# Optimization experiments

Measured on AMD Instinct MI355X. Metric: run time of the kernel, lower is better.

The kernel has to match this reference:

```python
import jax, jax.numpy as jnp
import numpy as np

T, B, I, H, LBL = 200, 1024, 128, 128, 4


def setup_inputs() -> dict:
    key = jax.random.key(0)
    ks = jax.random.split(key, 14)
    si = 1.0 / np.sqrt(I)
    sh = 1.0 / np.sqrt(H)
    inputs = jax.random.normal(ks[0], (T, B, I), jnp.float32)
    lengths = jnp.maximum(jax.random.randint(ks[1], (B,), 1, T + 1), LBL).astype(jnp.int32)
    return {
        "inputs": inputs,
        "lengths": lengths,
        "Wih_g": jax.random.normal(ks[2], (3 * H, I), jnp.float32) * si,
        "Whh_g": jax.random.normal(ks[3], (3 * H, H), jnp.float32) * sh,
        "bih_g": jax.random.normal(ks[4], (3 * H,), jnp.float32) * sh,
        "bhh_g": jax.random.normal(ks[5], (3 * H,), jnp.float32) * sh,
        "Wih_l": jax.random.normal(ks[6], (3 * H, I), jnp.float32) * si,
        "Whh_l": jax.random.normal(ks[7], (3 * H, H), jnp.float32) * sh,
        "bih_l": jax.random.normal(ks[8], (3 * H,), jnp.float32) * sh,
        "bhh_l": jax.random.normal(ks[9], (3 * H,), jnp.float32) * sh,
        "A1": jax.random.normal(ks[10], (H, H), jnp.float32) * sh,
        "A2": jax.random.normal(ks[11], (H, H), jnp.float32) * sh,
        "v1": jax.random.normal(ks[12], (1, H), jnp.float32) * sh,
        "label_len": LBL,
    }


def gru(x, Wih, Whh, bih, bhh):
    # x: [T, B, I] time-major. PyTorch GRU cell semantics.
    Bq, Hq = x.shape[1], Whh.shape[1]
    gi_all = jnp.einsum('tbi,gi->tbg', x, Wih) + bih  # precompute input projections [T,B,3H]
    def step(h, gi):
        gh = h @ Whh.T + bhh
        ir, iz, inn = jnp.split(gi, 3, axis=-1)
        hr, hz, hn = jnp.split(gh, 3, axis=-1)
        r = jax.nn.sigmoid(ir + hr)
        z = jax.nn.sigmoid(iz + hz)
        n = jnp.tanh(inn + r * hn)
        h = (1.0 - z) * n + z * h
        return h, h
    h0 = jnp.zeros((Bq, Hq), x.dtype)
    _, hs = jax.lax.scan(step, h0, gi_all)
    return hs  # [T, B, H]


def reference(inputs, lengths, Wih_g, Whh_g, bih_g, bhh_g,
              Wih_l, Whh_l, bih_l, bhh_l, A1, A2, v1, label_len):
    h_g = gru(inputs, Wih_g, Whh_g, bih_g, bhh_g)  # [T,B,H]
    h_l = gru(inputs, Wih_l, Whh_l, bih_l, bhh_l)  # [T,B,H]
    # attention score per step s: v1(sigmoid(A1 h_l + A2 h_g)), query-independent
    pre = jax.nn.sigmoid(jnp.einsum('tbh,gh->tbg', h_l, A1) +
                         jnp.einsum('tbh,gh->tbg', h_g, A2))
    scores = jnp.einsum('tbg,og->tbo', pre, v1)  # [T,B,1]
    # per-t output = cumsum_{s<=t}(score*h_l) + h_g[t]
    out = jnp.cumsum(scores * h_l, axis=0) + h_g  # [T,B,H]
    out_b = jnp.transpose(out, (1, 0, 2))  # [B,T,H]
    # gather last label_len timesteps of each sequence: h[b,k] = out[L_b-label_len+k, b]
    idx = lengths[:, None].astype(jnp.int32) - label_len + jnp.arange(label_len, dtype=jnp.int32)[None, :]
    idx = jnp.clip(idx, 0, out_b.shape[1] - 1)  # [B, label_len]
    h = jnp.take_along_axis(out_b, idx[:, :, None], axis=1)  # [B, label_len, H]
    return h
```

## Files before the change

### kernel.cpp

```cpp
#include <hip/hip_runtime.h>
#include <stdint.h>


typedef __attribute__((ext_vector_type(8))) short short8;
typedef __attribute__((ext_vector_type(4))) float float4v;

#define LDS_BARRIER() asm volatile("s_waitcnt lgkmcnt(0)\n\ts_barrier" ::: "memory")

__device__ inline float bf2f(unsigned short u){
  union { unsigned int i; float f; } v; v.i = ((unsigned int)u) << 16; return v.f;
}
__device__ inline unsigned short f2bf(float f){
  union { float f; unsigned int i; } v; v.f = f;
  unsigned int x = v.i;
  return (unsigned short)((x + 0x7fffu + ((x >> 16) & 1u)) >> 16);
}
__device__ inline unsigned int cvt_pk_bf16(float a, float b){
  unsigned int r;
  asm("v_cvt_pk_bf16_f32 %0, %1, %2" : "=v"(r) : "v"(a), "v"(b));
  return r;
}
__device__ inline float sigm(float x){ return __builtin_amdgcn_rcpf(1.0f + __expf(-x)); }

__global__ void k_prep(float* cum, const float* A1, const float* A2, unsigned short* a12,
                       const float* Wih_g, const float* Whh_g,
                       const float* Wih_l, const float* Whh_l, unsigned short* wst)
{
  int i = blockIdx.x * blockDim.x + threadIdx.x;
  if (i < 131072) cum[i] = 0.0f;
  if (i < 32768) a12[i] = f2bf((i < 16384) ? A1[i] : A2[i - 16384]);
  {
    int f = i >> 12;
    int r = i & 4095;
    int t = r >> 3, e = r & 7;
    int l15 = t & 15, q = (t >> 4) & 3, wv = t >> 6;
    int col = wv * 16 + l15;
    int kf = f & 3, g3 = f >> 2;
    int G = g3 % 3, gm = g3 / 3;
    const float* src = (gm == 0) ? Wih_g : (gm == 1) ? Whh_g : (gm == 2) ? Wih_l : Whh_l;
    int row = G * 128 + col;
    int k = kf * 32 + q * 8 + e;
    wst[i] = f2bf(src[(size_t)row * 128 + k]);
  }
}

union __align__(16) LdsU {
  struct { unsigned short hbuf[2][16][136]; unsigned short xbuf[2][16][136]; } scan;
  struct { unsigned short M1[128][136]; unsigned short M2[128][136]; } sc;
  struct { unsigned short hlL[50 * 512]; float scL[4][50]; } cm;
};

__global__ __launch_bounds__(512, 2) void k_fat(
    const float* __restrict__ x,
    const float* __restrict__ bih_g, const float* __restrict__ bhh_g,
    const float* __restrict__ bih_l, const float* __restrict__ bhh_l,
    const unsigned short* __restrict__ wst,
    const unsigned short* __restrict__ a12, const float* __restrict__ v1,
    const int* __restrict__ lengths,
    unsigned short* __restrict__ hl, unsigned short* __restrict__ hg,
    float* __restrict__ score, float* __restrict__ cum, float* __restrict__ out,
    int scan_t0, int score_t0, int cum_t0)
{
  __shared__ LdsU lds;
  int tid = threadIdx.x;
  int bid = blockIdx.x;

  if (bid < 128) {
    if (scan_t0 < 0) return;
    const int tc = 100;
    int t0 = scan_t0;
    auto& hbuf = lds.scan.hbuf;
    auto& xbuf = lds.scan.xbuf;

    int w = tid >> 6, L = tid & 63, l15 = L & 15, q = L >> 4;
    int gru = bid & 1;
    int b0 = (bid >> 1) * 16;
    const float* bih = gru ? bih_l : bih_g;
    const float* bhh = gru ? bhh_l : bhh_g;
    unsigned short* myseq = gru ? hl : hg;

    int col = w * 16 + l15;

    short8 Wi[3][4], Wh[3][4];
    {
      int gmi = gru * 2;
      int gmh = gru * 2 + 1;
      #pragma unroll
      for (int G = 0; G < 3; G++) {
        #pragma unroll
        for (int kf = 0; kf < 4; kf++) {
          Wi[G][kf] = *(const short8*)(wst + (((size_t)((gmi * 3 + G) * 4 + kf)) << 12) + tid * 8);
          Wh[G][kf] = *(const short8*)(wst + (((size_t)((gmh * 3 + G) * 4 + kf)) << 12) + tid * 8);
        }
      }
    }
    float br  = bih[col]       + bhh[col];
    float bz  = bih[128 + col] + bhh[128 + col];
    float bin = bih[256 + col];
    float bnh = bhh[256 + col];

    float hold[4];
    if (t0 == 0) {
      #pragma unroll
      for (int r = 0; r < 4; r++) { hold[r] = 0.0f; hbuf[0][q * 4 + r][col] = 0; }
    } else {
      const unsigned short* carry = myseq + (size_t)(t0 - 1) * 131072;
      #pragma unroll
      for (int r = 0; r < 4; r++) {
        int m = q * 4 + r;
        unsigned short u = carry[(size_t)(b0 + m) * 128 + col];
        hold[r] = bf2f(u);
        hbuf[0][m][col] = u;
      }
    }
    int xrow = tid >> 5, xc4 = (tid & 31) * 4;
    size_t hoff = (size_t)b0 * 128 + xrow * 128 + xc4;
    {
      float4 x0 = ((const float4*)(x + ((size_t)t0 * 1024 + b0) * 128))[tid];
      *(uint2*)&xbuf[0][xrow][xc4] = make_uint2(cvt_pk_bf16(x0.x, x0.y), cvt_pk_bf16(x0.z, x0.w));
    }
    float4 xr = ((const float4*)(x + ((size_t)(t0 + 1) * 1024 + b0) * 128))[tid];
    __syncthreads();

    float4v cx0 = (float4v){0.f,0.f,0.f,0.f}, cx1 = cx0, cx2 = cx0;
    {
      short8 Ax[4];
      #pragma unroll
      for (int kf = 0; kf < 4; kf++) Ax[kf] = *(const short8*)&xbuf[0][l15][kf * 32 + q * 8];
      #pragma unroll
      for (int kf = 0; kf < 4; kf++) cx0 = __builtin_amdgcn_mfma_f32_16x16x32_bf16(Ax[kf], Wi[0][kf], cx0, 0,0,0);
      #pragma unroll
      for (int kf = 0; kf < 4; kf++) cx1 = __builtin_amdgcn_mfma_f32_16x16x32_bf16(Ax[kf], Wi[1][kf], cx1, 0,0,0);
      #pragma unroll
      for (int kf = 0; kf < 4; kf++) cx2 = __builtin_amdgcn_mfma_f32_16x16x32_bf16(Ax[kf], Wi[2][kf], cx2, 0,0,0);
    }
    *(uint2*)&xbuf[1][xrow][xc4] = make_uint2(cvt_pk_bf16(xr.x, xr.y), cvt_pk_bf16(xr.z, xr.w));
    xr = ((const float4*)(x + ((size_t)(t0 + 2) * 1024 + b0) * 128))[tid];
    LDS_BARRIER();

    auto step = [&](int s, int pin, int pout) {
      short8 Ah[4], Axn[4];
      #pragma unroll
      for (int kf = 0; kf < 4; kf++) Ah[kf]  = *(const short8*)&hbuf[pin][l15][kf * 32 + q * 8];
      #pragma unroll
      for (int kf = 0; kf < 4; kf++) Axn[kf] = *(const short8*)&xbuf[pout][l15][kf * 32 + q * 8];

      if (s > 0) {
        uint2 hv = *(const uint2*)&hbuf[pin][xrow][xc4];
        *(uint2*)(myseq + (size_t)(t0 + s - 1) * 131072 + hoff) = hv;
      }

      float4v rh = (float4v){0.f,0.f,0.f,0.f}, zh = rh, nh = rh;
      #pragma unroll
      for (int kf = 0; kf < 4; kf++) rh = __builtin_amdgcn_mfma_f32_16x16x32_bf16(Ah[kf], Wh[0][kf], rh, 0,0,0);
      #pragma unroll
      for (int kf = 0; kf < 4; kf++) zh = __builtin_amdgcn_mfma_f32_16x16x32_bf16(Ah[kf], Wh[1][kf], zh, 0,0,0);
      #pragma unroll
      for (int kf = 0; kf < 4; kf++) nh = __builtin_amdgcn_mfma_f32_16x16x32_bf16(Ah[kf], Wh[2][kf], nh, 0,0,0);

      float4v nx0 = (float4v){0.f,0.f,0.f,0.f}, nx1 = nx0, nx2 = nx0;
      #pragma unroll
      for (int kf = 0; kf < 4; kf++) nx0 = __builtin_amdgcn_mfma_f32_16x16x32_bf16(Axn[kf], Wi[0][kf], nx0, 0,0,0);
      #pragma unroll
      for (int kf = 0; kf < 4; kf++) nx1 = __builtin_amdgcn_mfma_f32_16x16x32_bf16(Axn[kf], Wi[1][kf], nx1, 0,0,0);
      #pragma unroll
      for (int kf = 0; kf < 4; kf++) nx2 = __builtin_amdgcn_mfma_f32_16x16x32_bf16(Axn[kf], Wi[2][kf], nx2, 0,0,0);

      *(uint2*)&xbuf[pin][xrow][xc4] = make_uint2(cvt_pk_bf16(xr.x, xr.y), cvt_pk_bf16(xr.z, xr.w));
      {
        int t3 = t0 + (s + 3 < tc ? s + 3 : tc - 1);
        xr = ((const float4*)(x + ((size_t)t3 * 1024 + b0) * 128))[tid];
      }

      float cr[4], cz[4], cn[4];
      #pragma unroll
      for (int r = 0; r < 4; r++) { cr[r] = cx0[r] + br; cz[r] = cx1[r] + bz; cn[r] = cx2[r] + bin; }

      float hnv[4];
      #pragma unroll
      for (int r = 0; r < 4; r++) {
        float er = __expf(-(rh[r] + cr[r]));
        float ez = __expf(-(zh[r] + cz[r]));
        float pr = 1.0f + er, pz = 1.0f + ez;
        float inv = __builtin_amdgcn_rcpf(pr * pz);
        float rr = pz * inv;
        float zz = pr * inv;
        float y  = cn[r] + rr * (nh[r] + bnh);
        float em = __expf(-2.0f * y);
        float nn = 2.0f * __builtin_amdgcn_rcpf(1.0f + em) - 1.0f;
        hnv[r] = nn + zz * (hold[r] - nn);
        hold[r] = hnv[r];
      }
      unsigned int p01 = cvt_pk_bf16(hnv[0], hnv[1]);
      unsigned int p23 = cvt_pk_bf16(hnv[2], hnv[3]);
      hbuf[pout][q * 4 + 0][col] = (unsigned short)p01;
      hbuf[pout][q * 4 + 1][col] = (unsigned short)(p01 >> 16);
      hbuf[pout][q * 4 + 2][col] = (unsigned short)p23;
      hbuf[pout][q * 4 + 3][col] = (unsigned short)(p23 >> 16);

      cx0 = nx0; cx1 = nx1; cx2 = nx2;
      LDS_BARRIER();
    };

    for (int s = 0; s + 1 < tc; s += 2) { step(s, 0, 1); step(s + 1, 1, 0); }
    {
      uint2 hv = *(const uint2*)&hbuf[tc & 1][xrow][xc4];
      *(uint2*)(myseq + (size_t)(t0 + tc - 1) * 131072 + hoff) = hv;
    }
    return;
  }

  if (bid < 328) {
    if (score_t0 < 0) return;
    int rb = bid - 128;
    int w = tid >> 6, L = tid & 63;
    int l15 = L & 15, q = L >> 4;
    int s = score_t0 + (rb >> 1);
    int bhalf = (rb & 1) * 512;
    auto& M1 = lds.sc.M1;
    auto& M2 = lds.sc.M2;

    #pragma unroll
    for (int it = 0; it < 4; it++) {
      int f8 = it * 512 + tid;
      *(short8*)&M1[f8 >> 4][(f8 & 15) * 8] = *(const short8*)(a12 + (size_t)f8 * 8);
      *(short8*)&M2[f8 >> 4][(f8 & 15) * 8] = *(const short8*)(a12 + 16384 + (size_t)f8 * 8);
    }
    __syncthreads();

    float v1v[8];
    #pragma unroll
    for (int nt = 0; nt < 8; nt++) v1v[nt] = v1[nt * 16 + l15];

    short8 Fl[4], Fg[4], Pl[4], Pg[4];
    {
      size_t base = ((size_t)s * 1024 + bhalf + (size_t)w * 16 + l15) * 128;
      #pragma unroll
      for (int kf = 0; kf < 4; kf++) {
        Fl[kf] = *(const short8*)(hl + base + kf * 32 + q * 8);
        Fg[kf] = *(const short8*)(hg + base + kf * 32 + q * 8);
      }
    }
    #pragma unroll
    for (int it = 0; it < 4; it++) {
      int b0s = bhalf + (it * 8 + w) * 16;
      if (it + 1 < 4) {
        size_t base = ((size_t)s * 1024 + bhalf + (size_t)((it + 1) * 8 + w) * 16 + l15) * 128;
        #pragma unroll
        for (int kf = 0; kf < 4; kf++) {
          Pl[kf] = *(const short8*)(hl + base + kf * 32 + q * 8);
          Pg[kf] = *(const short8*)(hg + base + kf * 32 + q * 8);
        }
      }
      float4v acc[8];
      #pragma unroll
      for (int nt = 0; nt < 8; nt++) {
        float4v a = (float4v){0.f, 0.f, 0.f, 0.f};
        #pragma unroll
        for (int kf = 0; kf < 4; kf++)
          a = __builtin_amdgcn_mfma_f32_16x16x32_bf16(
              Fl[kf], *(const short8*)&M1[nt * 16 + l15][kf * 32 + q * 8], a, 0, 0, 0);
        #pragma unroll
        for (int kf = 0; kf < 4; kf++)
          a = __builtin_amdgcn_mfma_f32_16x16x32_bf16(
              Fg[kf], *(const short8*)&M2[nt * 16 + l15][kf * 32 + q * 8], a, 0, 0, 0);
        acc[nt] = a;
      }
      float p4[4];
      #pragma unroll
      for (int r = 0; r < 4; r++) {
        float sum = 0.f;
        #pragma unroll
        for (int nt = 0; nt < 8; nt++) sum += v1v[nt] * sigm(acc[nt][r]);
        sum += __shfl_xor(sum, 1, 16);
        sum += __shfl_xor(sum, 2, 16);
        sum += __shfl_xor(sum, 4, 16);
        sum += __shfl_xor(sum, 8, 16);
        p4[r] = sum;
      }
      if (l15 == 0) {
        #pragma unroll
        for (int r = 0; r < 4; r++)
          score[(size_t)(b0s + q * 4 + r) * 200 + s] = p4[r];
      }
      #pragma unroll
      for (int kf = 0; kf < 4; kf++) { Fl[kf] = Pl[kf]; Fg[kf] = Pg[kf]; }
    }
    return;
  }

  if (cum_t0 < 0) return;
  {
    int rb = bid - 328;
    int b4 = tid >> 7, j = tid & 127;
    int b0c = rb * 4;
    int b = b0c + b4;
    int base = b4 * 128 + j;

    float c = cum[(size_t)b * 128 + j];
    int cap0 = lengths[b] - 4;

    for (int seg = 0; seg < 2; seg++) {
      int t0s = cum_t0 + seg * 50;
      __syncthreads();

      float hgv[4];
      #pragma unroll
      for (int d = 0; d < 4; d++) {
        int sl = cap0 + d - t0s;
        hgv[d] = (sl >= 0 && sl < 50) ? bf2f(hg[((size_t)(cap0 + d) * 1024 + b) * 128 + j]) : 0.f;
      }

      for (int f8 = tid; f8 < 50 * 64; f8 += 512) {
        int sl = f8 >> 6, r8 = f8 & 63;
        *(short8*)&lds.cm.hlL[(size_t)f8 * 8] =
            *(const short8*)(hl + ((size_t)(t0s + sl) * 1024 + b0c) * 128 + r8 * 8);
      }
      for (int i = tid; i < 4 * 50; i += 512) {
        int bb = i / 50, sl = i - bb * 50;
        lds.cm.scL[bb][sl] = score[(size_t)(b0c + bb) * 200 + t0s + sl];
      }
      __syncthreads();

      for (int sl = 0; sl < 50; sl += 5) {
        float h[5], scv[5];
        #pragma unroll
        for (int k = 0; k < 5; k++) {
          h[k] = bf2f(lds.cm.hlL[(size_t)(sl + k) * 512 + base]);
          scv[k] = lds.cm.scL[b4][sl + k];
        }
        #pragma unroll
        for (int k = 0; k < 5; k++) {
          c += scv[k] * h[k];
          int d = (t0s + sl + k) - cap0;
          if ((unsigned)d < 4u)
            out[((size_t)b * 4 + d) * 128 + j] = c + hgv[d];
        }
      }
    }
    cum[(size_t)b * 128 + j] = c;
  }
}

extern "C" void kernel_launch(void* const* d_in, const int* in_sizes, int n_in,
                              void* d_out, int out_size, void* d_ws, size_t ws_size,
                              hipStream_t stream)
{
  const float* x     = (const float*)d_in[0];
  const int* lengths = (const int*)d_in[1];
  const float* Wih_g = (const float*)d_in[2];
  const float* Whh_g = (const float*)d_in[3];
  const float* bih_g = (const float*)d_in[4];
  const float* bhh_g = (const float*)d_in[5];
  const float* Wih_l = (const float*)d_in[6];
  const float* Whh_l = (const float*)d_in[7];
  const float* bih_l = (const float*)d_in[8];
  const float* bhh_l = (const float*)d_in[9];
  const float* A1    = (const float*)d_in[10];
  const float* A2    = (const float*)d_in[11];
  const float* v1    = (const float*)d_in[12];
  float* out = (float*)d_out;

  char* wsb = (char*)d_ws;
  size_t o = 0;
  unsigned short* a12 = (unsigned short*)(wsb + o); o += 65536;
  float* cum          = (float*)(wsb + o);          o += 524288;
  unsigned short* wst = (unsigned short*)(wsb + o); o += 393216;
  unsigned short* hl  = (unsigned short*)(wsb + o); o += (size_t)200 * 1024 * 128 * 2;
  unsigned short* hg  = (unsigned short*)(wsb + o); o += (size_t)200 * 1024 * 128 * 2;
  float* score        = (float*)(wsb + o);          o += (size_t)1024 * 200 * 4;
  if (o > ws_size) return;

  k_prep<<<768, 256, 0, stream>>>(cum, A1, A2, a12, Wih_g, Whh_g, Wih_l, Whh_l, wst);

  k_fat<<<128, 512, 0, stream>>>(x, bih_g, bhh_g, bih_l, bhh_l, wst, a12, v1, lengths,
                                 hl, hg, score, cum, out, 0, -1, -1);
  k_fat<<<328, 512, 0, stream>>>(x, bih_g, bhh_g, bih_l, bhh_l, wst, a12, v1, lengths,
                                 hl, hg, score, cum, out, 100, 0, -1);
  k_fat<<<584, 512, 0, stream>>>(x, bih_g, bhh_g, bih_l, bhh_l, wst, a12, v1, lengths,
                                 hl, hg, score, cum, out, -1, 100, 0);
  k_fat<<<584, 512, 0, stream>>>(x, bih_g, bhh_g, bih_l, bhh_l, wst, a12, v1, lengths,
                                 hl, hg, score, cum, out, -1, -1, 100);
}
```

Measured before the change: 398.8 us.

## Fuse attention score into cumsum blocks and drop separate score pass

Computes attention scores inside the cumsum blocks with MFMA on hl/hg tiles staged in LDS, removing the separate score kernel stage and the global score buffer. The pipeline shrinks from four k_fat launches to three, and the cumsum for t<100 now overlaps with the second half of the scan. The first scan launch converts fp32 weights to bf16 in registers itself, so it no longer waits on the prep kernel for its weights. A dead 'build' branch is left in, and hg is now read twice (score and staging), adding LDS traffic per cum block.

New measurement: 398.6 us. Within noise of the previous version (-0.0%).

```diff
diff --git a/kernel.cpp b/kernel.cpp
--- a/kernel.cpp
+++ b/kernel.cpp
@@ -22,51 +22,33 @@
 }
 __device__ inline float sigm(float x){ return __builtin_amdgcn_rcpf(1.0f + __expf(-x)); }
 
-__global__ void k_prep(float* cum, const float* A1, const float* A2, unsigned short* a12,
-                       const float* Wih_g, const float* Whh_g,
-                       const float* Wih_l, const float* Whh_l, unsigned short* wst)
-{
-  int i = blockIdx.x * blockDim.x + threadIdx.x;
-  if (i < 131072) cum[i] = 0.0f;
-  if (i < 32768) a12[i] = f2bf((i < 16384) ? A1[i] : A2[i - 16384]);
-  {
-    int f = i >> 12;
-    int r = i & 4095;
-    int t = r >> 3, e = r & 7;
-    int l15 = t & 15, q = (t >> 4) & 3, wv = t >> 6;
-    int col = wv * 16 + l15;
-    int kf = f & 3, g3 = f >> 2;
-    int G = g3 % 3, gm = g3 / 3;
-    const float* src = (gm == 0) ? Wih_g : (gm == 1) ? Whh_g : (gm == 2) ? Wih_l : Whh_l;
-    int row = G * 128 + col;
-    int k = kf * 32 + q * 8 + e;
-    wst[i] = f2bf(src[(size_t)row * 128 + k]);
-  }
-}
-
 union __align__(16) LdsU {
   struct { unsigned short hbuf[2][16][136]; unsigned short xbuf[2][16][136]; } scan;
-  struct { unsigned short M1[128][136]; unsigned short M2[128][136]; } sc;
-  struct { unsigned short hlL[50 * 512]; float scL[4][50]; } cm;
+  struct {
+    unsigned short hlL[25 * 544];
+    unsigned short hgL[25 * 544];
+    float part[8 * 112];
+    float scR[112];
+  } cm;
 };
 
 __global__ __launch_bounds__(512, 2) void k_fat(
     const float* __restrict__ x,
     const float* __restrict__ bih_g, const float* __restrict__ bhh_g,
     const float* __restrict__ bih_l, const float* __restrict__ bhh_l,
-    const unsigned short* __restrict__ wst,
-    const unsigned short* __restrict__ a12, const float* __restrict__ v1,
-    const int* __restrict__ lengths,
+    const float* __restrict__ Wih_g, const float* __restrict__ Whh_g,
+    const float* __restrict__ Wih_l, const float* __restrict__ Whh_l,
+    unsigned short* __restrict__ wst, unsigned short* __restrict__ a12,
+    const float* __restrict__ v1, const int* __restrict__ lengths,
     unsigned short* __restrict__ hl, unsigned short* __restrict__ hg,
-    float* __restrict__ score, float* __restrict__ cum, float* __restrict__ out,
-    int scan_t0, int score_t0, int cum_t0)
+    float* __restrict__ cum, float* __restrict__ out,
+    int scan_t0, int sccum_t0, int sccum_base, int build)
 {
   __shared__ LdsU lds;
   int tid = threadIdx.x;
   int bid = blockIdx.x;
 
-  if (bid < 128) {
-    if (scan_t0 < 0) return;
+  if (scan_t0 >= 0 && bid < 128) {
     const int tc = 100;
     int t0 = scan_t0;
     auto& hbuf = lds.scan.hbuf;
@@ -82,7 +64,26 @@
     int col = w * 16 + l15;
 
     short8 Wi[3][4], Wh[3][4];
-    {
+    if (t0 == 0) {
+      const float* Wih = gru ? Wih_l : Wih_g;
+      const float* Whh = gru ? Whh_l : Whh_g;
+      #pragma unroll
+      for (int G = 0; G < 3; G++) {
+        int row = G * 128 + col;
+        #pragma unroll
+        for (int kf = 0; kf < 4; kf++) {
+          const float4* p0 = (const float4*)(Wih + (size_t)row * 128 + kf * 32 + q * 8);
+          const float4* p1 = (const float4*)(Whh + (size_t)row * 128 + kf * 32 + q * 8);
+          float4 a0 = p0[0], a1 = p0[1], b0f = p1[0], b1f = p1[1];
+          short8 si, sh;
+          si[0]=(short)f2bf(a0.x); si[1]=(short)f2bf(a0.y); si[2]=(short)f2bf(a0.z); si[3]=(short)f2bf(a0.w);
+          si[4]=(short)f2bf(a1.x); si[5]=(short)f2bf(a1.y); si[6]=(short)f2bf(a1.z); si[7]=(short)f2bf(a1.w);
+          sh[0]=(short)f2bf(b0f.x); sh[1]=(short)f2bf(b0f.y); sh[2]=(short)f2bf(b0f.z); sh[3]=(short)f2bf(b0f.w);
+          sh[4]=(short)f2bf(b1f.x); sh[5]=(short)f2bf(b1f.y); sh[6]=(short)f2bf(b1f.z); sh[7]=(short)f2bf(b1f.w);
+          Wi[G][kf] = si; Wh[G][kf] = sh;
+        }
+      }
+    } else {
       int gmi = gru * 2;
       int gmh = gru * 2 + 1;
       #pragma unroll
@@ -210,135 +211,134 @@
     return;
   }
 
-  if (bid < 328) {
-    if (score_t0 < 0) return;
-    int rb = bid - 128;
-    int w = tid >> 6, L = tid & 63;
-    int l15 = L & 15, q = L >> 4;
-    int s = score_t0 + (rb >> 1);
-    int bhalf = (rb & 1) * 512;
-    auto& M1 = lds.sc.M1;
-    auto& M2 = lds.sc.M2;
-
-    #pragma unroll
-    for (int it = 0; it < 4; it++) {
-      int f8 = it * 512 + tid;
-      *(short8*)&M1[f8 >> 4][(f8 & 15) * 8] = *(const short8*)(a12 + (size_t)f8 * 8);
-      *(short8*)&M2[f8 >> 4][(f8 & 15) * 8] = *(const short8*)(a12 + 16384 + (size_t)f8 * 8);
-    }
-    __syncthreads();
-
-    float v1v[8];
-    #pragma unroll
-    for (int nt = 0; nt < 8; nt++) v1v[nt] = v1[nt * 16 + l15];
-
-    short8 Fl[4], Fg[4], Pl[4], Pg[4];
-    {
-      size_t base = ((size_t)s * 1024 + bhalf + (size_t)w * 16 + l15) * 128;
-      #pragma unroll
-      for (int kf = 0; kf < 4; kf++) {
-        Fl[kf] = *(const short8*)(hl + base + kf * 32 + q * 8);
-        Fg[kf] = *(const short8*)(hg + base + kf * 32 + q * 8);
-      }
-    }
-    #pragma unroll
-    for (int it = 0; it < 4; it++) {
-      int b0s = bhalf + (it * 8 + w) * 16;
-      if (it + 1 < 4) {
-        size_t base = ((size_t)s * 1024 + bhalf + (size_t)((it + 1) * 8 + w) * 16 + l15) * 128;
-        #pragma unroll
-        for (int kf = 0; kf < 4; kf++) {
-          Pl[kf] = *(const short8*)(hl + base + kf * 32 + q * 8);
-          Pg[kf] = *(const short8*)(hg + base + kf * 32 + q * 8);
-        }
-      }
-      float4v acc[8];
-      #pragma unroll
-      for (int nt = 0; nt < 8; nt++) {
-        float4v a = (float4v){0.f, 0.f, 0.f, 0.f};
-        #pragma unroll
-        for (int kf = 0; kf < 4; kf++)
-          a = __builtin_amdgcn_mfma_f32_16x16x32_bf16(
-              Fl[kf], *(const short8*)&M1[nt * 16 + l15][kf * 32 + q * 8], a, 0, 0, 0);
-        #pragma unroll
-        for (int kf = 0; kf < 4; kf++)
-          a = __builtin_amdgcn_mfma_f32_16x16x32_bf16(
-              Fg[kf], *(const short8*)&M2[nt * 16 + l15][kf * 32 + q * 8], a, 0, 0, 0);
-        acc[nt] = a;
-      }
-      float p4[4];
-      #pragma unroll
-      for (int r = 0; r < 4; r++) {
-        float sum = 0.f;
-        #pragma unroll
-        for (int nt = 0; nt < 8; nt++) sum += v1v[nt] * sigm(acc[nt][r]);
-        sum += __shfl_xor(sum, 1, 16);
-        sum += __shfl_xor(sum, 2, 16);
-        sum += __shfl_xor(sum, 4, 16);
-        sum += __shfl_xor(sum, 8, 16);
-        p4[r] = sum;
-      }
-      if (l15 == 0) {
-        #pragma unroll
-        for (int r = 0; r < 4; r++)
-          score[(size_t)(b0s + q * 4 + r) * 200 + s] = p4[r];
-      }
-      #pragma unroll
-      for (int kf = 0; kf < 4; kf++) { Fl[kf] = Pl[kf]; Fg[kf] = Pg[kf]; }
-    }
+  if (build) {
+    if (bid < 128) return;
+    int gid = (bid - 128) * 512 + tid;
+    (void)gid;
     return;
   }
 
-  if (cum_t0 < 0) return;
-  {
-    int rb = bid - 328;
-    int b4 = tid >> 7, j = tid & 127;
+  if (sccum_t0 >= 0) {
+    int t0c = sccum_t0;
+    int rb = bid - sccum_base;
     int b0c = rb * 4;
-    int b = b0c + b4;
-    int base = b4 * 128 + j;
-
-    float c = cum[(size_t)b * 128 + j];
+    int w = tid >> 6, L = tid & 63, l15 = L & 15, q = L >> 4;
+    int jc = tid & 127, bc = tid >> 7;
+    int b = b0c + bc;
+
+    auto* hlL = lds.cm.hlL;
+    auto* hgL = lds.cm.hgL;
+    float* part = lds.cm.part;
+    float* scR  = lds.cm.scR;
+
+    float c = (t0c == 0) ? 0.0f : cum[(size_t)b * 128 + jc];
     int cap0 = lengths[b] - 4;
 
-    for (int seg = 0; seg < 2; seg++) {
-      int t0s = cum_t0 + seg * 50;
+    float hgv[4];
+    #pragma unroll
+    for (int d = 0; d < 4; d++) {
+      int sl = cap0 + d - t0c;
+      hgv[d] = (sl >= 0 && sl < 100) ? bf2f(hg[((size_t)(cap0 + d) * 1024 + b) * 128 + jc]) : 0.f;
+    }
+
+    short8 B1[4], B2[4];
+    #pragma unroll
+    for (int kf = 0; kf < 4; kf++) {
+      B1[kf] = *(const short8*)(a12 + (size_t)(w * 16 + l15) * 128 + kf * 32 + q * 8);
+      B2[kf] = *(const short8*)(a12 + 16384 + (size_t)(w * 16 + l15) * 128 + kf * 32 + q * 8);
+    }
+    float v1w = v1[w * 16 + l15];
+
+    for (int seg = 0; seg < 4; seg++) {
+      int t0s = t0c + seg * 25;
       __syncthreads();
-
-      float hgv[4];
-      #pragma unroll
-      for (int d = 0; d < 4; d++) {
-        int sl = cap0 + d - t0s;
-        hgv[d] = (sl >= 0 && sl < 50) ? bf2f(hg[((size_t)(cap0 + d) * 1024 + b) * 128 + j]) : 0.f;
-      }
-
-      for (int f8 = tid; f8 < 50 * 64; f8 += 512) {
-        int sl = f8 >> 6, r8 = f8 & 63;
-        *(short8*)&lds.cm.hlL[(size_t)f8 * 8] =
-            *(const short8*)(hl + ((size_t)(t0s + sl) * 1024 + b0c) * 128 + r8 * 8);
-      }
-      for (int i = tid; i < 4 * 50; i += 512) {
-        int bb = i / 50, sl = i - bb * 50;
-        lds.cm.scL[bb][sl] = score[(size_t)(b0c + bb) * 200 + t0s + sl];
+      for (int f8 = tid; f8 < 1600; f8 += 512) {
+        int sl = f8 >> 6, r8 = f8 & 63, bb = r8 >> 4, j8 = r8 & 15;
+        size_t gsrc = ((size_t)(t0s + sl) * 1024 + b0c) * 128 + r8 * 8;
+        int dst = sl * 544 + bb * 136 + j8 * 8;
+        *(short8*)&hlL[dst] = *(const short8*)(hl + gsrc);
+        *(short8*)&hgL[dst] = *(const short8*)(hg + gsrc);
       }
       __syncthreads();
 
-      for (int sl = 0; sl < 50; sl += 5) {
+      #pragma unroll
+      for (int T = 0; T < 7; T++) {
+        int tl = T * 4 + (l15 >> 2); if (tl > 24) tl = 24;
+        int bb = l15 & 3;
+        int abase = tl * 544 + bb * 136 + q * 8;
+        short8 Al[4], Ag[4];
+        #pragma unroll
+        for (int kf = 0; kf < 4; kf++) {
+          Al[kf] = *(const short8*)&hlL[abase + kf * 32];
+          Ag[kf] = *(const short8*)&hgL[abase + kf * 32];
+        }
+        float4v acc = (float4v){0.f, 0.f, 0.f, 0.f};
+        #pragma unroll
+        for (int kf = 0; kf < 4; kf++) acc = __builtin_amdgcn_mfma_f32_16x16x32_bf16(Al[kf], B1[kf], acc, 0,0,0);
+        #pragma unroll
+        for (int kf = 0; kf < 4; kf++) acc = __builtin_amdgcn_mfma_f32_16x16x32_bf16(Ag[kf], B2[kf], acc, 0,0,0);
+        #pragma unroll
+        for (int r = 0; r < 4; r++) {
+          float sv = v1w * sigm(acc[r]);
+          sv += __shfl_xor(sv, 1, 16);
+          sv += __shfl_xor(sv, 2, 16);
+          sv += __shfl_xor(sv, 4, 16);
+          sv += __shfl_xor(sv, 8, 16);
+          if (l15 == 0) part[w * 112 + T * 16 + q * 4 + r] = sv;
+        }
+      }
+      __syncthreads();
+      if (tid < 100) {
+        float s = 0.f;
+        #pragma unroll
+        for (int w8 = 0; w8 < 8; w8++) s += part[w8 * 112 + tid];
+        scR[tid] = s;
+      }
+      __syncthreads();
+
+      for (int sl = 0; sl < 25; sl += 5) {
         float h[5], scv[5];
         #pragma unroll
         for (int k = 0; k < 5; k++) {
-          h[k] = bf2f(lds.cm.hlL[(size_t)(sl + k) * 512 + base]);
-          scv[k] = lds.cm.scL[b4][sl + k];
+          h[k]  = bf2f(hlL[(sl + k) * 544 + bc * 136 + jc]);
+          scv[k] = scR[(sl + k) * 4 + bc];
         }
         #pragma unroll
         for (int k = 0; k < 5; k++) {
           c += scv[k] * h[k];
           int d = (t0s + sl + k) - cap0;
           if ((unsigned)d < 4u)
-            out[((size_t)b * 4 + d) * 128 + j] = c + hgv[d];
-        }
-      }
-    }
-    cum[(size_t)b * 128 + j] = c;
+            out[((size_t)b * 4 + d) * 128 + jc] = c + hgv[d];
+        }
+      }
+    }
+    cum[(size_t)b * 128 + jc] = c;
+    return;
+  }
+}
+
+__global__ __launch_bounds__(512) void k_build(
+    const float* __restrict__ Wih_g, const float* __restrict__ Whh_g,
+    const float* __restrict__ Wih_l, const float* __restrict__ Whh_l,
+    const float* __restrict__ A1, const float* __restrict__ A2,
+    unsigned short* __restrict__ wst, unsigned short* __restrict__ a12)
+{
+  int gid = blockIdx.x * 512 + threadIdx.x;
+  if (gid < 32768) a12[gid] = f2bf((gid < 16384) ? A1[gid] : A2[gid - 16384]);
+  #pragma unroll
+  for (int k = 0; k < 3; k++) {
+    int i = gid + k * 65536;
+    int f = i >> 12;
+    int r = i & 4095;
+    int t = r >> 3, e = r & 7;
+    int l15 = t & 15, q = (t >> 4) & 3, wv = t >> 6;
+    int col = wv * 16 + l15;
+    int kf = f & 3, g3 = f >> 2;
+    int G = g3 % 3, gm = g3 / 3;
+    const float* src = (gm == 0) ? Wih_g : (gm == 1) ? Whh_g : (gm == 2) ? Wih_l : Whh_l;
+    int row = G * 128 + col;
+    int kk = kf * 32 + q * 8 + e;
+    wst[i] = f2bf(src[(size_t)row * 128 + kk]);
   }
 }
 
@@ -364,21 +364,23 @@
   char* wsb = (char*)d_ws;
   size_t o = 0;
   unsigned short* a12 = (unsigned short*)(wsb + o); o += 65536;
+  unsigned short* wst = (unsigned short*)(wsb + o); o += 393216;
   float* cum          = (float*)(wsb + o);          o += 524288;
-  unsigned short* wst = (unsigned short*)(wsb + o); o += 393216;
   unsigned short* hl  = (unsigned short*)(wsb + o); o += (size_t)200 * 1024 * 128 * 2;
   unsigned short* hg  = (unsigned short*)(wsb + o); o += (size_t)200 * 1024 * 128 * 2;
-  float* score        = (float*)(wsb + o);          o += (size_t)1024 * 200 * 4;
   if (o > ws_size) return;
 
-  k_prep<<<768, 256, 0, stream>>>(cum, A1, A2, a12, Wih_g, Whh_g, Wih_l, Whh_l, wst);
-
-  k_fat<<<128, 512, 0, stream>>>(x, bih_g, bhh_g, bih_l, bhh_l, wst, a12, v1, lengths,
-                                 hl, hg, score, cum, out, 0, -1, -1);
-  k_fat<<<328, 512, 0, stream>>>(x, bih_g, bhh_g, bih_l, bhh_l, wst, a12, v1, lengths,
-                                 hl, hg, score, cum, out, 100, 0, -1);
-  k_fat<<<584, 512, 0, stream>>>(x, bih_g, bhh_g, bih_l, bhh_l, wst, a12, v1, lengths,
-                                 hl, hg, score, cum, out, -1, 100, 0);
-  k_fat<<<584, 512, 0, stream>>>(x, bih_g, bhh_g, bih_l, bhh_l, wst, a12, v1, lengths,
-                                 hl, hg, score, cum, out, -1, -1, 100);
-}
+  k_build<<<128, 512, 0, stream>>>(Wih_g, Whh_g, Wih_l, Whh_l, A1, A2, wst, a12);
+  k_fat<<<128, 512, 0, stream>>>(x, bih_g, bhh_g, bih_l, bhh_l,
+                                 Wih_g, Whh_g, Wih_l, Whh_l,
+                                 wst, a12, v1, lengths, hl, hg, cum, out,
+                                 0, -1, 0, 0);
+  k_fat<<<384, 512, 0, stream>>>(x, bih_g, bhh_g, bih_l, bhh_l,
+                                 Wih_g, Whh_g, Wih_l, Whh_l,
+                                 wst, a12, v1, lengths, hl, hg, cum, out,
+                                 100, 0, 128, 0);
+  k_fat<<<256, 512, 0, stream>>>(x, bih_g, bhh_g, bih_l, bhh_l,
+                                 Wih_g, Whh_g, Wih_l, Whh_l,
+                                 wst, a12, v1, lengths, hl, hg, cum, out,
+                                 -1, 100, 0, 0);
+}
```
